# Optimization experiments

Measured on AMD Instinct MI355X. Metric: run time of the kernel, lower is better.

## Reference

```python
import jax, jax.numpy as jnp
import numpy as np

EMBED = 128
HEADS = 8
DEPTH = EMBED // HEADS
N, L = 32, 4096


def setup_inputs() -> dict:
    key = jax.random.key(0)
    ks = jax.random.split(key, 11)
    s = 1.0 / np.sqrt(EMBED)
    inp = {
        "values": jax.random.normal(ks[0], (N, L, EMBED), jnp.float32),
        "keys": jax.random.normal(ks[1], (N, L, EMBED), jnp.float32),
        "queries": jax.random.normal(ks[2], (N, L, EMBED), jnp.float32),
        "Wv": jax.random.normal(ks[3], (EMBED, EMBED), jnp.float32) * s,
        "bv": jnp.zeros((EMBED,), jnp.float32),
        "Wk": jax.random.normal(ks[4], (EMBED, EMBED), jnp.float32) * s,
        "bk": jnp.zeros((EMBED,), jnp.float32),
        "Wq": jax.random.normal(ks[5], (EMBED, EMBED), jnp.float32) * s,
        "bq": jnp.zeros((EMBED,), jnp.float32),
        "Wo": jax.random.normal(ks[6], (EMBED, EMBED), jnp.float32) * s,
        "bo": jnp.zeros((EMBED,), jnp.float32),
    }
    return inp


def reference(values, keys, queries, Wv, bv, Wk, bk, Wq, bq, Wo, bo):
    n, l, e = queries.shape
    h, d = HEADS, DEPTH
    # Linear projections (torch Linear: x @ W^T + b; here W stored as (in, out))
    v = (values @ Wv + bv).reshape(n, l, h, d)
    k = (keys @ Wk + bk).reshape(n, l, h, d)
    q = (queries @ Wq + bq).reshape(n, l, h, d)
    # Original einsum 'nbhd,mbhd->nhbm' attends across the BATCH axis at each
    # sequence position; the chunk loop over positions never mixes positions,
    # so it is equivalent to one vectorized einsum over all positions t.
    scores = jnp.einsum('nthd,mthd->nhtm', q, k)  # [N, H, L, N]
    attn = jax.nn.softmax(scores, axis=-1)
    out = jnp.einsum('nhtm,mthd->nthd', attn, v).reshape(n, l, e)
    return out @ Wo + bo
```

## Files before the change

kernel.cpp:

```cpp
#include <hip/hip_runtime.h>

#define LSEQ 4096

typedef __bf16 bf16x8 __attribute__((ext_vector_type(8)));
typedef float f32x16 __attribute__((ext_vector_type(16)));

union FU { unsigned u[4]; uint4 u4; bf16x8 v; };

__device__ __forceinline__ unsigned short bfb(float f) {
  __bf16 h = (__bf16)f;
  return __builtin_bit_cast(unsigned short, h);
}
__device__ __forceinline__ unsigned pk2(float a, float b) {
  return (unsigned)bfb(a) | ((unsigned)bfb(b) << 16);
}
__device__ __forceinline__ void xchg(unsigned P0, unsigned P1, unsigned P2, unsigned P3,
                                     const int hi, unsigned o[4]) {
  const unsigned sA = hi ? P0 : P2, sB = hi ? P1 : P3;
  const unsigned rA = __shfl_xor(sA, 32), rB = __shfl_xor(sB, 32);
  o[0] = hi ? rA : P0; o[1] = hi ? rB : P1;
  o[2] = hi ? P2 : rA; o[3] = hi ? P3 : rB;
}

__global__ __launch_bounds__(64) void repack(
    const float* __restrict__ Wv, const float* __restrict__ bv,
    const float* __restrict__ Wk, const float* __restrict__ bk,
    const float* __restrict__ Wq, const float* __restrict__ bq,
    const float* __restrict__ Wo, const float* __restrict__ bo,
    uint4* __restrict__ ws) {
  const int b = blockIdx.x;
  const int ks = b % 9, nt = (b / 9) & 3, m = b / 36;
  const float* Ws[4] = {Wv, Wk, Wq, Wo};
  const float* Bs[4] = {bv, bk, bq, bo};
  const int l = threadIdx.x, l31 = l & 31, hi = l >> 5;
  FU f;
  if (ks < 8) {
#pragma unroll
    for (int e = 0; e < 4; ++e) {
      const float a = Ws[m][(ks * 16 + hi * 8 + 2 * e) * 128 + nt * 32 + l31];
      const float c = Ws[m][(ks * 16 + hi * 8 + 2 * e + 1) * 128 + nt * 32 + l31];
      f.u[e] = pk2(a, c);
    }
  } else {
    f.u[0] = (hi == 0) ? (unsigned)bfb(Bs[m][nt * 32 + l31]) : 0u;
    f.u[1] = 0; f.u[2] = 0; f.u[3] = 0;
  }
  ws[b * 64 + l] = f.u4;
}

__global__ __launch_bounds__(256, 4) void fused_mha(
    const float* __restrict__ Xv, const float* __restrict__ Xk, const float* __restrict__ Xq,
    const uint4* __restrict__ wf4, float* __restrict__ out) {
  __shared__ uint4 xlds[3 * 8 * 64];
  __shared__ uint4 olds[8 * 64];
  const int tid = threadIdx.x;
  const int t = blockIdx.x;

  {
    const int r = tid >> 3, ksc = tid & 7;
    const float* Xs[3] = {Xv, Xk, Xq};
#pragma unroll
    for (int tau = 0; tau < 3; ++tau) {
      const float4* p4 = reinterpret_cast<const float4*>(
          Xs[tau] + ((long)r * LSEQ + t) * 128 + ksc * 16);
      const float4 a = p4[0], b = p4[1], c = p4[2], d = p4[3];
      FU lo, hb;
      lo.u[0] = pk2(a.x, a.y); lo.u[1] = pk2(a.z, a.w);
      lo.u[2] = pk2(b.x, b.y); lo.u[3] = pk2(b.z, b.w);
      hb.u[0] = pk2(c.x, c.y); hb.u[1] = pk2(c.z, c.w);
      hb.u[2] = pk2(d.x, d.y); hb.u[3] = pk2(d.z, d.w);
      xlds[(tau * 8 + ksc) * 64 + (r ^ ksc)] = lo.u4;
      xlds[(tau * 8 + ksc) * 64 + ((r ^ ksc) | 32)] = hb.u4;
    }
  }
  __syncthreads();

  const int wid = tid >> 6, l = tid & 63;
  const int nt = wid, l31 = l & 31, hi = l >> 5;
  FU cf;
  cf.u[0] = hi ? 0u : 0x00003F80u; cf.u[1] = 0; cf.u[2] = 0; cf.u[3] = 0;

  unsigned vpk[8];
  FU kf[2], qf[2];

  {
    f32x16 acc = {};
#pragma unroll
    for (int ks = 0; ks < 8; ++ks) {
      FU xf; xf.u4 = xlds[(0 * 8 + ks) * 64 + (l ^ ks)];
      FU wf; wf.u4 = wf4[((0 * 4 + nt) * 9 + ks) * 64 + l];
      acc = __builtin_amdgcn_mfma_f32_32x32x16_bf16(xf.v, wf.v, acc, 0, 0, 0);
    }
    FU wb; wb.u4 = wf4[((0 * 4 + nt) * 9 + 8) * 64 + l];
    acc = __builtin_amdgcn_mfma_f32_32x32x16_bf16(cf.v, wb.v, acc, 0, 0, 0);
#pragma unroll
    for (int jv = 0; jv < 8; ++jv) vpk[jv] = pk2(acc[2 * jv], acc[2 * jv + 1]);
  }
  {
    f32x16 acc = {};
#pragma unroll
    for (int ks = 0; ks < 8; ++ks) {
      FU xf; xf.u4 = xlds[(1 * 8 + ks) * 64 + (l ^ ks)];
      FU wf; wf.u4 = wf4[((1 * 4 + nt) * 9 + ks) * 64 + l];
      acc = __builtin_amdgcn_mfma_f32_32x32x16_bf16(wf.v, xf.v, acc, 0, 0, 0);
    }
    FU wb; wb.u4 = wf4[((1 * 4 + nt) * 9 + 8) * 64 + l];
    acc = __builtin_amdgcn_mfma_f32_32x32x16_bf16(wb.v, cf.v, acc, 0, 0, 0);
#pragma unroll
    for (int ch = 0; ch < 2; ++ch) {
      const int c8 = ch * 8;
      xchg(pk2(acc[c8 + 0], acc[c8 + 1]), pk2(acc[c8 + 2], acc[c8 + 3]),
           pk2(acc[c8 + 4], acc[c8 + 5]), pk2(acc[c8 + 6], acc[c8 + 7]), hi, kf[ch].u);
    }
  }
  {
    f32x16 acc = {};
#pragma unroll
    for (int ks = 0; ks < 8; ++ks) {
      FU xf; xf.u4 = xlds[(2 * 8 + ks) * 64 + (l ^ ks)];
      FU wf; wf.u4 = wf4[((2 * 4 + nt) * 9 + ks) * 64 + l];
      acc = __builtin_amdgcn_mfma_f32_32x32x16_bf16(wf.v, xf.v, acc, 0, 0, 0);
    }
    FU wb; wb.u4 = wf4[((2 * 4 + nt) * 9 + 8) * 64 + l];
    acc = __builtin_amdgcn_mfma_f32_32x32x16_bf16(wb.v, cf.v, acc, 0, 0, 0);
#pragma unroll
    for (int ch = 0; ch < 2; ++ch) {
      const int c8 = ch * 8;
      xchg(pk2(acc[c8 + 0], acc[c8 + 1]), pk2(acc[c8 + 2], acc[c8 + 3]),
           pk2(acc[c8 + 4], acc[c8 + 5]), pk2(acc[c8 + 6], acc[c8 + 7]), hi, qf[ch].u);
    }
  }

  {
    FU vm0, vm1, vs0, vs1;
    xchg(vpk[0], vpk[1], vpk[2], vpk[3], hi, vm0.u);
    xchg(vpk[4], vpk[5], vpk[6], vpk[7], hi, vm1.u);
#pragma unroll
    for (int i = 0; i < 4; ++i) {
      vs0.u[i] = __shfl_xor(vm0.u[i], 16);
      vs1.u[i] = __shfl_xor(vm1.u[i], 16);
    }
#pragma unroll
    for (int ch = 0; ch < 2; ++ch) {
      const int h = nt * 2 + ch;
      const bool own = ((l31 >> 4) == ch);
      f32x16 zz = {};
      f32x16 S = __builtin_amdgcn_mfma_f32_32x32x16_bf16(kf[ch].v, qf[ch].v, zz, 0, 0, 0);
      float mx = S[0];
#pragma unroll
      for (int r = 1; r < 16; ++r) mx = fmaxf(mx, S[r]);
      mx = fmaxf(mx, __shfl_xor(mx, 32));
      float p[16], sum = 0.f;
#pragma unroll
      for (int r = 0; r < 16; ++r) {
        p[r] = exp2f((S[r] - mx) * 1.44269504089f);
        sum += p[r];
      }
      sum += __shfl_xor(sum, 32);
      const float inv = 1.0f / sum;
      FU pf0, pf1;
      xchg(pk2(p[0], p[1]), pk2(p[2], p[3]), pk2(p[4], p[5]), pk2(p[6], p[7]), hi, pf0.u);
      xchg(pk2(p[8], p[9]), pk2(p[10], p[11]), pk2(p[12], p[13]), pk2(p[14], p[15]), hi, pf1.u);
      FU v0, v1;
#pragma unroll
      for (int i = 0; i < 4; ++i) {
        v0.u[i] = own ? vm0.u[i] : vs0.u[i];
        v1.u[i] = own ? vm1.u[i] : vs1.u[i];
      }
      f32x16 z2 = {};
      f32x16 Ot = __builtin_amdgcn_mfma_f32_32x32x16_bf16(v0.v, pf0.v, z2, 0, 0, 0);
      Ot = __builtin_amdgcn_mfma_f32_32x32x16_bf16(v1.v, pf1.v, Ot, 0, 0, 0);
      FU ofr;
      xchg(pk2(Ot[0] * inv, Ot[1] * inv), pk2(Ot[2] * inv, Ot[3] * inv),
           pk2(Ot[4] * inv, Ot[5] * inv), pk2(Ot[6] * inv, Ot[7] * inv), hi, ofr.u);
      olds[h * 64 + l] = ofr.u4;
    }
  }
  __syncthreads();

  {
    f32x16 acc = {};
#pragma unroll
    for (int h = 0; h < 8; ++h) {
      FU of; of.u4 = olds[h * 64 + l];
      FU wf; wf.u4 = wf4[((3 * 4 + nt) * 9 + h) * 64 + l];
      acc = __builtin_amdgcn_mfma_f32_32x32x16_bf16(of.v, wf.v, acc, 0, 0, 0);
    }
    FU wb; wb.u4 = wf4[((3 * 4 + nt) * 9 + 8) * 64 + l];
    acc = __builtin_amdgcn_mfma_f32_32x32x16_bf16(cf.v, wb.v, acc, 0, 0, 0);
#pragma unroll
    for (int r = 0; r < 16; ++r) {
      const int n = (r & 3) + ((r >> 2) << 3) + (hi << 2);
      out[((long)n * LSEQ + t) * 128 + nt * 32 + l31] = acc[r];
    }
  }
}

extern "C" void kernel_launch(void* const* d_in, const int* in_sizes, int n_in,
                              void* d_out, int out_size, void* d_ws, size_t ws_size,
                              hipStream_t stream) {
  const float* values  = (const float*)d_in[0];
  const float* keys    = (const float*)d_in[1];
  const float* queries = (const float*)d_in[2];
  const float* Wv = (const float*)d_in[3];
  const float* bv = (const float*)d_in[4];
  const float* Wk = (const float*)d_in[5];
  const float* bk = (const float*)d_in[6];
  const float* Wq = (const float*)d_in[7];
  const float* bq = (const float*)d_in[8];
  const float* Wo = (const float*)d_in[9];
  const float* bo = (const float*)d_in[10];

  repack<<<dim3(144), dim3(64), 0, stream>>>(Wv, bv, Wk, bk, Wq, bq, Wo, bo,
                                             (uint4*)d_ws);
  fused_mha<<<dim3(LSEQ), dim3(256), 0, stream>>>(
      values, keys, queries, (const uint4*)d_ws, (float*)d_out);
}
```

Baseline: 64.64 us.

## Prefetch weight fragments into registers with double-buffered loads across projections

Weight fragments for the V and K projections are loaded into registers before the X staging and barrier, and the Q and output weights are loaded one stage ahead into alternating register buffers. This hides global-load latency for the weights behind the MFMA work of the previous stage. It raises register pressure by about 72 extra VGPRs, and to make room the launch bound drops from 4 to 3 blocks per SIMD group, which can lower occupancy.

New measurement: 65.67 us. About the same (+1.6%).

```diff
diff --git a/kernel.cpp b/kernel.cpp
--- a/kernel.cpp
+++ b/kernel.cpp
@@ -20,6 +20,13 @@
   const unsigned rA = __shfl_xor(sA, 32), rB = __shfl_xor(sB, 32);
   o[0] = hi ? rA : P0; o[1] = hi ? rB : P1;
   o[2] = hi ? P2 : rA; o[3] = hi ? P3 : rB;
+}
+
+__device__ __forceinline__ void loadW(const uint4* __restrict__ wf4, int mat, int nt,
+                                      int l, FU w[9]) {
+#pragma unroll
+  for (int ks = 0; ks < 9; ++ks)
+    w[ks].u4 = wf4[((mat * 4 + nt) * 9 + ks) * 64 + l];
 }
 
 __global__ __launch_bounds__(64) void repack(
@@ -48,13 +55,19 @@
   ws[b * 64 + l] = f.u4;
 }
 
-__global__ __launch_bounds__(256, 4) void fused_mha(
+__global__ __launch_bounds__(256, 3) void fused_mha(
     const float* __restrict__ Xv, const float* __restrict__ Xk, const float* __restrict__ Xq,
     const uint4* __restrict__ wf4, float* __restrict__ out) {
   __shared__ uint4 xlds[3 * 8 * 64];
   __shared__ uint4 olds[8 * 64];
   const int tid = threadIdx.x;
   const int t = blockIdx.x;
+  const int wid = tid >> 6, l = tid & 63;
+  const int nt = wid, l31 = l & 31, hi = l >> 5;
+
+  FU wfA[9], wfB[9];
+  loadW(wf4, 0, nt, l, wfA);
+  loadW(wf4, 1, nt, l, wfB);
 
   {
     const int r = tid >> 3, ksc = tid & 7;
@@ -75,8 +88,6 @@
   }
   __syncthreads();
 
-  const int wid = tid >> 6, l = tid & 63;
-  const int nt = wid, l31 = l & 31, hi = l >> 5;
   FU cf;
   cf.u[0] = hi ? 0u : 0x00003F80u; cf.u[1] = 0; cf.u[2] = 0; cf.u[3] = 0;
 
@@ -88,24 +99,23 @@
 #pragma unroll
     for (int ks = 0; ks < 8; ++ks) {
       FU xf; xf.u4 = xlds[(0 * 8 + ks) * 64 + (l ^ ks)];
-      FU wf; wf.u4 = wf4[((0 * 4 + nt) * 9 + ks) * 64 + l];
-      acc = __builtin_amdgcn_mfma_f32_32x32x16_bf16(xf.v, wf.v, acc, 0, 0, 0);
-    }
-    FU wb; wb.u4 = wf4[((0 * 4 + nt) * 9 + 8) * 64 + l];
-    acc = __builtin_amdgcn_mfma_f32_32x32x16_bf16(cf.v, wb.v, acc, 0, 0, 0);
+      acc = __builtin_amdgcn_mfma_f32_32x32x16_bf16(xf.v, wfA[ks].v, acc, 0, 0, 0);
+    }
+    acc = __builtin_amdgcn_mfma_f32_32x32x16_bf16(cf.v, wfA[8].v, acc, 0, 0, 0);
 #pragma unroll
     for (int jv = 0; jv < 8; ++jv) vpk[jv] = pk2(acc[2 * jv], acc[2 * jv + 1]);
   }
+
+  loadW(wf4, 2, nt, l, wfA);
+
   {
     f32x16 acc = {};
 #pragma unroll
     for (int ks = 0; ks < 8; ++ks) {
       FU xf; xf.u4 = xlds[(1 * 8 + ks) * 64 + (l ^ ks)];
-      FU wf; wf.u4 = wf4[((1 * 4 + nt) * 9 + ks) * 64 + l];
-      acc = __builtin_amdgcn_mfma_f32_32x32x16_bf16(wf.v, xf.v, acc, 0, 0, 0);
-    }
-    FU wb; wb.u4 = wf4[((1 * 4 + nt) * 9 + 8) * 64 + l];
-    acc = __builtin_amdgcn_mfma_f32_32x32x16_bf16(wb.v, cf.v, acc, 0, 0, 0);
+      acc = __builtin_amdgcn_mfma_f32_32x32x16_bf16(wfB[ks].v, xf.v, acc, 0, 0, 0);
+    }
+    acc = __builtin_amdgcn_mfma_f32_32x32x16_bf16(wfB[8].v, cf.v, acc, 0, 0, 0);
 #pragma unroll
     for (int ch = 0; ch < 2; ++ch) {
       const int c8 = ch * 8;
@@ -113,16 +123,17 @@
            pk2(acc[c8 + 4], acc[c8 + 5]), pk2(acc[c8 + 6], acc[c8 + 7]), hi, kf[ch].u);
     }
   }
+
+  loadW(wf4, 3, nt, l, wfB);
+
   {
     f32x16 acc = {};
 #pragma unroll
     for (int ks = 0; ks < 8; ++ks) {
       FU xf; xf.u4 = xlds[(2 * 8 + ks) * 64 + (l ^ ks)];
-      FU wf; wf.u4 = wf4[((2 * 4 + nt) * 9 + ks) * 64 + l];
-      acc = __builtin_amdgcn_mfma_f32_32x32x16_bf16(wf.v, xf.v, acc, 0, 0, 0);
-    }
-    FU wb; wb.u4 = wf4[((2 * 4 + nt) * 9 + 8) * 64 + l];
-    acc = __builtin_amdgcn_mfma_f32_32x32x16_bf16(wb.v, cf.v, acc, 0, 0, 0);
+      acc = __builtin_amdgcn_mfma_f32_32x32x16_bf16(wfA[ks].v, xf.v, acc, 0, 0, 0);
+    }
+    acc = __builtin_amdgcn_mfma_f32_32x32x16_bf16(wfA[8].v, cf.v, acc, 0, 0, 0);
 #pragma unroll
     for (int ch = 0; ch < 2; ++ch) {
       const int c8 = ch * 8;
@@ -183,11 +194,9 @@
 #pragma unroll
     for (int h = 0; h < 8; ++h) {
       FU of; of.u4 = olds[h * 64 + l];
-      FU wf; wf.u4 = wf4[((3 * 4 + nt) * 9 + h) * 64 + l];
-      acc = __builtin_amdgcn_mfma_f32_32x32x16_bf16(of.v, wf.v, acc, 0, 0, 0);
-    }
-    FU wb; wb.u4 = wf4[((3 * 4 + nt) * 9 + 8) * 64 + l];
-    acc = __builtin_amdgcn_mfma_f32_32x32x16_bf16(cf.v, wb.v, acc, 0, 0, 0);
+      acc = __builtin_amdgcn_mfma_f32_32x32x16_bf16(of.v, wfB[h].v, acc, 0, 0, 0);
+    }
+    acc = __builtin_amdgcn_mfma_f32_32x32x16_bf16(cf.v, wfB[8].v, acc, 0, 0, 0);
 #pragma unroll
     for (int r = 0; r < 16; ++r) {
       const int n = (r & 3) + ((r >> 2) << 3) + (hi << 2);
```
